# Kernel optimization log

Hardware: AMD Instinct MI355X
Metric: run time of the kernel (lower is better)

## Reference

```python
import jax, jax.numpy as jnp
import numpy as np

NDIGIT = 10
DIM_IN = 256
DIM_OUT = 784
BATCH = 16384


def setup_inputs() -> dict:
    key = jax.random.key(0)
    k_theta, k_label, k_W = jax.random.split(key, 3)
    theta = jax.random.normal(k_theta, (BATCH, DIM_IN), dtype=jnp.float32)
    label = jax.random.randint(k_label, (BATCH,), 0, NDIGIT, dtype=jnp.int32)
    # xavier_uniform for each (dim_out, dim_in) matrix
    limit = float(np.sqrt(6.0 / (DIM_IN + DIM_OUT)))
    megaW = jax.random.uniform(k_W, (NDIGIT, DIM_OUT, DIM_IN), dtype=jnp.float32,
                               minval=-limit, maxval=limit)
    megab = jnp.zeros((NDIGIT, DIM_OUT), dtype=jnp.float32)
    return {"theta": theta, "label": label, "megaW": megaW, "megab": megab}


def reference(theta, label, megaW, megab):
    # Dense compute across all 10 digit experts (matches torch.bmm over repeated theta)
    # added: [b, ndigit, dim_out]
    added = jnp.einsum('ndi,bi->bnd', megaW, theta) + megab[None, :, :]
    # Select the expert output per example by label (vector_gather)
    selected = jnp.take_along_axis(added, label[:, None, None].astype(jnp.int32), axis=1)[:, 0, :]
    probs = jax.nn.sigmoid(selected)
    return probs
```

## Files before the change

### kernel.cpp

```cpp
#include <hip/hip_runtime.h>
#include <hip/hip_bf16.h>

#define NDIGIT 10
#define DIM_IN 256
#define DIM_OUT 784
#define BATCH 16384
#define BM 64
#define BN 112
#define NCB 7
#define MAX_MT (BATCH / BM + NDIGIT)
#define GEMM_BLOCKS (MAX_MT * NCB)
#define QBYTES 14336

#define WS_IDX 1024
#define WS_WBF_BYTES 69632
#define WS_TH_BYTES (WS_WBF_BYTES + 2007040 * 2)
#define WS_NEED_OLD (WS_TH_BYTES)
#define WS_NEED_NEW (WS_TH_BYTES + BATCH * DIM_IN * 2)

typedef __attribute__((ext_vector_type(4))) float f32x4;
typedef __attribute__((ext_vector_type(8))) short bf16x8;

__device__ __forceinline__ short f2bf(float f) {
    union { float f; unsigned u; } c; c.f = f;
    unsigned u = c.u;
    u += 0x7fffu + ((u >> 16) & 1u);
    return (short)(u >> 16);
}

__device__ __forceinline__ void gload16(const void* gp, void* lp) {
    __builtin_amdgcn_global_load_lds(
        (const __attribute__((address_space(1))) void*)gp,
        (__attribute__((address_space(3))) void*)lp, 16, 0, 0);
}

__global__ void prep_k(const float* __restrict__ megaW,
                       const int* __restrict__ label,
                       int* __restrict__ wsi,
                       short* __restrict__ wbf) {
    int b = blockIdx.x, t = threadIdx.x;
    if (b < 980) {
        int base = b * 2048 + t * 8;
        f32x4 v0 = *(const f32x4*)(megaW + base);
        f32x4 v1 = *(const f32x4*)(megaW + base + 4);
        bf16x8 o;
        o[0] = f2bf(v0[0]); o[1] = f2bf(v0[1]); o[2] = f2bf(v0[2]); o[3] = f2bf(v0[3]);
        o[4] = f2bf(v1[0]); o[5] = f2bf(v1[1]); o[6] = f2bf(v1[2]); o[7] = f2bf(v1[3]);
        *(bf16x8*)(wbf + base) = o;
    } else {
        __shared__ int h[NDIGIT];
        int j = b - 980;
        if (t < NDIGIT) h[t] = 0;
        __syncthreads();
        int i0 = j * 512;
        atomicAdd(&h[label[i0 + t]], 1);
        atomicAdd(&h[label[i0 + 256 + t]], 1);
        __syncthreads();
        if (t < NDIGIT) wsi[64 + j * 16 + t] = h[t];
    }
}

__global__ void scatter2_k(const int* __restrict__ label, int* __restrict__ wsi) {
    __shared__ int tot[NDIGIT], bef[NDIGIT], base[NDIGIT + 1], cur[NDIGIT];
    int j = blockIdx.x, t = threadIdx.x;
    if (t < NDIGIT) {
        int s = 0, sb = 0;
        for (int jj = 0; jj < 32; ++jj) {
            int v = wsi[64 + jj * 16 + t];
            s += v;
            if (jj < j) sb += v;
        }
        tot[t] = s; bef[t] = sb;
    }
    __syncthreads();
    if (t == 0) {
        int off = 0;
        for (int g = 0; g < NDIGIT; ++g) { base[g] = off; off += tot[g]; }
        base[NDIGIT] = off;
    }
    __syncthreads();
    if (t < NDIGIT) cur[t] = base[t] + bef[t];
    __syncthreads();
    int i = j * 512 + t;
    int g = label[i];
    int r = atomicAdd(&cur[g], 1);
    wsi[WS_IDX + r] = i;
    if (j == 0 && t == 0) {
        int off = 0, toff = 0;
        for (int g2 = 0; g2 < NDIGIT; ++g2) {
            wsi[g2] = off; wsi[12 + g2] = toff;
            off += tot[g2]; toff += (tot[g2] + BM - 1) / BM;
        }
        wsi[10] = off; wsi[22] = toff; wsi[24] = toff;
    }
}

__global__ void gth_k(const float* __restrict__ theta,
                      const int* __restrict__ wsi,
                      short* __restrict__ thsort) {
    int gid = blockIdx.x * 256 + threadIdx.x;
    int r = gid >> 5;
    int c8 = (gid & 31) << 3;
    int src = wsi[WS_IDX + r];
    const float* p = theta + (size_t)src * DIM_IN + c8;
    f32x4 v0 = *(const f32x4*)p;
    f32x4 v1 = *(const f32x4*)(p + 4);
    bf16x8 o;
    o[0] = f2bf(v0[0]); o[1] = f2bf(v0[1]); o[2] = f2bf(v0[2]); o[3] = f2bf(v0[3]);
    o[4] = f2bf(v1[0]); o[5] = f2bf(v1[1]); o[6] = f2bf(v1[2]); o[7] = f2bf(v1[3]);
    *(bf16x8*)(thsort + (size_t)r * DIM_IN + c8) = o;
}

__device__ __forceinline__ void stage_q(const char* Wcb, int q, char* Bq, int tid) {
#pragma unroll
    for (int it = 0; it < 4; ++it) {
        int chunk = it * 256 + tid;
        if (chunk >= 896) chunk -= 128;
        int lbyte = chunk << 4;
        int L = lbyte ^ ((((lbyte >> 7) & 7)) << 4);
        int row = L >> 7, koff = L & 127;
        gload16(Wcb + row * 512 + q * 128 + koff, Bq + lbyte);
    }
}

#define COMPUTE(Q, BUF) do { \
    _Pragma("unroll") \
    for (int ksl = 0; ksl < 2; ++ksl) { \
        _Pragma("unroll") \
        for (int ns = 0; ns < NCB; ++ns) { \
            int n = ns * 16 + r16; \
            int byte = (n << 7) + (ksl << 6) + (kg << 4); \
            byte ^= (n & 7) << 4; \
            bf16x8 bfr = *(const bf16x8*)((const char*)(BUF) + byte); \
            acc[ns] = __builtin_amdgcn_mfma_f32_16x16x32_bf16(a[(Q) * 2 + ksl], bfr, acc[ns], 0, 0, 0); \
        } \
    } \
} while (0)

__launch_bounds__(256, 4)
__global__ void moe_gemm5_k(const short* __restrict__ thsort,
                            const float* __restrict__ megab,
                            const int* __restrict__ wsi,
                            const short* __restrict__ wbf,
                            float* __restrict__ out) {
    __shared__ char Bs0[QBYTES];
    __shared__ char Bs1[QBYTES];

    int Bid = blockIdx.x;
    const int q8 = GEMM_BLOCKS / 8, r8 = GEMM_BLOCKS % 8;
    int xcd = Bid & 7, slot = Bid >> 3;
    int w = (xcd < r8 ? xcd * (q8 + 1) : r8 * (q8 + 1) + (xcd - r8) * q8) + slot;
    int mt = w / NCB, cb = w % NCB;

    int total = wsi[24];
    if (mt >= total) return;

    int g = 0;
    while (mt >= wsi[12 + g + 1]) ++g;
    int lt    = mt - wsi[12 + g];
    int start = wsi[g];
    int cnt   = wsi[g + 1] - start;
    int row0  = lt * BM;
    int rc    = min(BM, cnt - row0);

    int tid = threadIdx.x;
    int wv = tid >> 6, l = tid & 63, r16 = l & 15, kg = l >> 4;

    int arow = start + row0 + wv * 16 + r16;
    if (arow > BATCH - 1) arow = BATCH - 1;
    const short* Ar = thsort + (size_t)arow * DIM_IN + kg * 8;
    bf16x8 a[8];
#pragma unroll
    for (int ks = 0; ks < 8; ++ks)
        a[ks] = *(const bf16x8*)(Ar + ks * 32);

    const int* idxlist = wsi + WS_IDX + start + row0;
    int rbase = wv * 16 + kg * 4;
    int orow[4];
#pragma unroll
    for (int j = 0; j < 4; ++j)
        orow[j] = (rbase + j < rc) ? idxlist[rbase + j] : -1;

    const char* Wcb = (const char*)(wbf + ((size_t)g * DIM_OUT + (size_t)cb * BN) * DIM_IN);

    stage_q(Wcb, 0, Bs0, tid);
    stage_q(Wcb, 1, Bs1, tid);

    f32x4 acc[NCB];
#pragma unroll
    for (int ns = 0; ns < NCB; ++ns) acc[ns] = (f32x4){0.f, 0.f, 0.f, 0.f};

    asm volatile("s_waitcnt vmcnt(4)" ::: "memory");
    __builtin_amdgcn_s_barrier();
    __builtin_amdgcn_sched_barrier(0);

    COMPUTE(0, Bs0);
    asm volatile("s_waitcnt lgkmcnt(0)" ::: "memory");
    __builtin_amdgcn_s_barrier();
    stage_q(Wcb, 2, Bs0, tid);
    asm volatile("s_waitcnt vmcnt(4)" ::: "memory");
    __builtin_amdgcn_s_barrier();
    __builtin_amdgcn_sched_barrier(0);

    COMPUTE(1, Bs1);
    asm volatile("s_waitcnt lgkmcnt(0)" ::: "memory");
    __builtin_amdgcn_s_barrier();
    stage_q(Wcb, 3, Bs1, tid);
    asm volatile("s_waitcnt vmcnt(4)" ::: "memory");
    __builtin_amdgcn_s_barrier();
    __builtin_amdgcn_sched_barrier(0);

    COMPUTE(2, Bs0);
    asm volatile("s_waitcnt lgkmcnt(0) vmcnt(0)" ::: "memory");
    __builtin_amdgcn_s_barrier();
    __builtin_amdgcn_sched_barrier(0);

    COMPUTE(3, Bs1);

    const float* bg = megab + (size_t)g * DIM_OUT + (size_t)cb * BN;
#pragma unroll
    for (int ns = 0; ns < NCB; ++ns) {
        int nloc = ns * 16 + r16;
        float bias = bg[nloc];
#pragma unroll
        for (int j = 0; j < 4; ++j) {
            if (orow[j] >= 0) {
                float x = acc[ns][j] + bias;
                out[(size_t)orow[j] * DIM_OUT + cb * BN + nloc] = 1.0f / (1.0f + __expf(-x));
            }
        }
    }
}

__launch_bounds__(256, 4)
__global__ void moe_gemm4_k(const float* __restrict__ theta,
                            const float* __restrict__ megab,
                            const int* __restrict__ wsi,
                            const short* __restrict__ wbf,
                            float* __restrict__ out) {
    __shared__ short Bsf[BN * 128];
    int Bid = blockIdx.x;
    const int q8 = GEMM_BLOCKS / 8, r8 = GEMM_BLOCKS % 8;
    int xcd = Bid & 7, slot = Bid >> 3;
    int w = (xcd < r8 ? xcd * (q8 + 1) : r8 * (q8 + 1) + (xcd - r8) * q8) + slot;
    int mt = w / NCB, cb = w % NCB;
    int total = wsi[24];
    if (mt >= total) return;
    int g = 0;
    while (mt >= wsi[12 + g + 1]) ++g;
    int lt    = mt - wsi[12 + g];
    int start = wsi[g];
    int cnt   = wsi[g + 1] - start;
    int row0  = lt * BM;
    int rc    = min(BM, cnt - row0);
    int tid = threadIdx.x;
    int wv = tid >> 6, l = tid & 63, r16 = l & 15, kg = l >> 4;
    const char* Wcb = (const char*)(wbf + ((size_t)g * DIM_OUT + (size_t)cb * BN) * DIM_IN);
#pragma unroll
    for (int it = 0; it < 7; ++it) {
        int lbyte = (it * 256 + tid) << 4;
        int L = lbyte ^ (((lbyte >> 8) & 7) << 4);
        int srcoff = ((L >> 8) << 9) + (L & 255);
        gload16(Wcb + srcoff, (char*)Bsf + lbyte);
    }
    const int* idxlist = wsi + WS_IDX + start + row0;
    int mloc = wv * 16 + r16;
    int asrc = (mloc < rc) ? idxlist[mloc] : idxlist[0];
    const float* Arow = (const float*)0;
    Arow = theta + (size_t)asrc * DIM_IN;
    bf16x8 a[8];
#pragma unroll
    for (int ks = 0; ks < 8; ++ks) {
        int k0 = ks * 32 + kg * 8;
        f32x4 v0 = *(const f32x4*)(Arow + k0);
        f32x4 v1 = *(const f32x4*)(Arow + k0 + 4);
        bf16x8 af;
        af[0] = f2bf(v0[0]); af[1] = f2bf(v0[1]);
        af[2] = f2bf(v0[2]); af[3] = f2bf(v0[3]);
        af[4] = f2bf(v1[0]); af[5] = f2bf(v1[1]);
        af[6] = f2bf(v1[2]); af[7] = f2bf(v1[3]);
        a[ks] = af;
    }
    f32x4 acc[NCB];
#pragma unroll
    for (int ns = 0; ns < NCB; ++ns) acc[ns] = (f32x4){0.f, 0.f, 0.f, 0.f};
    __syncthreads();
#pragma unroll
    for (int ks = 0; ks < 4; ++ks)
#pragma unroll
        for (int ns = 0; ns < NCB; ++ns) {
            int n = ns * 16 + r16;
            int byte = (n << 8) + (ks << 6) + (kg << 4);
            byte ^= (n & 7) << 4;
            bf16x8 b = *(const bf16x8*)((const char*)Bsf + byte);
            acc[ns] = __builtin_amdgcn_mfma_f32_16x16x32_bf16(a[ks], b, acc[ns], 0, 0, 0);
        }
    __syncthreads();
#pragma unroll
    for (int it = 0; it < 7; ++it) {
        int lbyte = (it * 256 + tid) << 4;
        int L = lbyte ^ (((lbyte >> 8) & 7) << 4);
        int srcoff = ((L >> 8) << 9) + (L & 255) + 256;
        gload16(Wcb + srcoff, (char*)Bsf + lbyte);
    }
    __syncthreads();
#pragma unroll
    for (int ks = 0; ks < 4; ++ks)
#pragma unroll
        for (int ns = 0; ns < NCB; ++ns) {
            int n = ns * 16 + r16;
            int byte = (n << 8) + (ks << 6) + (kg << 4);
            byte ^= (n & 7) << 4;
            bf16x8 b = *(const bf16x8*)((const char*)Bsf + byte);
            acc[ns] = __builtin_amdgcn_mfma_f32_16x16x32_bf16(a[4 + ks], b, acc[ns], 0, 0, 0);
        }
    const float* bg = megab + (size_t)g * DIM_OUT + (size_t)cb * BN;
    int rbase = wv * 16 + kg * 4;
    int orow[4];
#pragma unroll
    for (int j = 0; j < 4; ++j)
        orow[j] = (rbase + j < rc) ? idxlist[rbase + j] : -1;
#pragma unroll
    for (int ns = 0; ns < NCB; ++ns) {
        int nloc = ns * 16 + r16;
        float bias = bg[nloc];
#pragma unroll
        for (int j = 0; j < 4; ++j) {
            if (orow[j] >= 0) {
                float x = acc[ns][j] + bias;
                out[(size_t)orow[j] * DIM_OUT + cb * BN + nloc] = 1.0f / (1.0f + __expf(-x));
            }
        }
    }
}

extern "C" void kernel_launch(void* const* d_in, const int* in_sizes, int n_in,
                              void* d_out, int out_size, void* d_ws, size_t ws_size,
                              hipStream_t stream) {
    const float* theta = (const float*)d_in[0];
    const int*   label = (const int*)d_in[1];
    const float* megaW = (const float*)d_in[2];
    const float* megab = (const float*)d_in[3];
    float* out = (float*)d_out;
    int* wsi = (int*)d_ws;
    short* wbf = (short*)((char*)d_ws + WS_WBF_BYTES);

    prep_k    <<<1012, 256, 0, stream>>>(megaW, label, wsi, wbf);
    scatter2_k<<<32, 512, 0, stream>>>(label, wsi);

    if (ws_size >= (size_t)WS_NEED_NEW) {
        short* thsort = (short*)((char*)d_ws + WS_TH_BYTES);
        gth_k     <<<2048, 256, 0, stream>>>(theta, wsi, thsort);
        moe_gemm5_k<<<GEMM_BLOCKS, 256, 0, stream>>>(thsort, megab, wsi, wbf, out);
    } else {
        moe_gemm4_k<<<GEMM_BLOCKS, 256, 0, stream>>>(theta, megab, wsi, wbf, out);
    }
}
```

Measured before the change: 47.19 us.

## Precompute per-tile descriptors and simplify GEMM LDS staging schedule

The scatter kernel now writes a packed per-M-tile descriptor (start row, row count, expert id), so each GEMM block does one load instead of a serial search over expert tile offsets. The GEMM kernel drops the hand-tuned interleaved waitcnt and barrier pipeline. It now stages two K-quarters, computes both, syncs, then stages and computes the last two. The weight staging is issued before the A-fragment loads to overlap them. This trades finer-grained load/compute overlap for fewer barriers and simpler code, with some risk of exposed memory latency in the second half.

```diff
diff --git a/kernel.cpp b/kernel.cpp
--- a/kernel.cpp
+++ b/kernel.cpp
@@ -9,14 +9,14 @@
 #define BN 112
 #define NCB 7
 #define MAX_MT (BATCH / BM + NDIGIT)
-#define GEMM_BLOCKS (MAX_MT * NCB)
-#define QBYTES 14336
+#define G_BLOCKS (MAX_MT * NCB)
+#define QB 14336
 
 #define WS_IDX 1024
+#define WS_DESC 600
 #define WS_WBF_BYTES 69632
 #define WS_TH_BYTES (WS_WBF_BYTES + 2007040 * 2)
-#define WS_NEED_OLD (WS_TH_BYTES)
-#define WS_NEED_NEW (WS_TH_BYTES + BATCH * DIM_IN * 2)
+#define WS_NEED (WS_TH_BYTES + BATCH * DIM_IN * 2)
 
 typedef __attribute__((ext_vector_type(4))) float f32x4;
 typedef __attribute__((ext_vector_type(8))) short bf16x8;
@@ -61,7 +61,7 @@
 }
 
 __global__ void scatter2_k(const int* __restrict__ label, int* __restrict__ wsi) {
-    __shared__ int tot[NDIGIT], bef[NDIGIT], base[NDIGIT + 1], cur[NDIGIT];
+    __shared__ int tot[NDIGIT], bef[NDIGIT], base[NDIGIT + 1], cur[NDIGIT], toff[NDIGIT + 1];
     int j = blockIdx.x, t = threadIdx.x;
     if (t < NDIGIT) {
         int s = 0, sb = 0;
@@ -74,25 +74,34 @@
     }
     __syncthreads();
     if (t == 0) {
-        int off = 0;
-        for (int g = 0; g < NDIGIT; ++g) { base[g] = off; off += tot[g]; }
-        base[NDIGIT] = off;
+        int off = 0, tf = 0;
+        for (int g = 0; g < NDIGIT; ++g) {
+            base[g] = off; toff[g] = tf;
+            off += tot[g]; tf += (tot[g] + BM - 1) / BM;
+        }
+        base[NDIGIT] = off; toff[NDIGIT] = tf;
     }
     __syncthreads();
     if (t < NDIGIT) cur[t] = base[t] + bef[t];
+    if (j == 0) {
+        int ptotal = toff[NDIGIT];
+        for (int p = t; p < ptotal; p += 512) {
+            int g2 = 0;
+            while (p >= toff[g2 + 1]) ++g2;
+            int row0 = (p - toff[g2]) * BM;
+            int rcv = tot[g2] - row0; if (rcv > BM) rcv = BM;
+            wsi[WS_DESC + p] = (base[g2] + row0) | (rcv << 14) | (g2 << 21);
+        }
+        if (t < NDIGIT) { wsi[t] = base[t]; wsi[12 + t] = toff[t]; }
+        if (t == 0) {
+            wsi[10] = base[NDIGIT]; wsi[22] = toff[NDIGIT]; wsi[24] = toff[NDIGIT];
+        }
+    }
     __syncthreads();
     int i = j * 512 + t;
     int g = label[i];
     int r = atomicAdd(&cur[g], 1);
     wsi[WS_IDX + r] = i;
-    if (j == 0 && t == 0) {
-        int off = 0, toff = 0;
-        for (int g2 = 0; g2 < NDIGIT; ++g2) {
-            wsi[g2] = off; wsi[12 + g2] = toff;
-            off += tot[g2]; toff += (tot[g2] + BM - 1) / BM;
-        }
-        wsi[10] = off; wsi[22] = toff; wsi[24] = toff;
-    }
 }
 
 __global__ void gth_k(const float* __restrict__ theta,
@@ -123,31 +132,31 @@
     }
 }
 
-#define COMPUTE(Q, BUF) do { \
-    _Pragma("unroll") \
-    for (int ksl = 0; ksl < 2; ++ksl) { \
-        _Pragma("unroll") \
-        for (int ns = 0; ns < NCB; ++ns) { \
-            int n = ns * 16 + r16; \
-            int byte = (n << 7) + (ksl << 6) + (kg << 4); \
-            byte ^= (n & 7) << 4; \
-            bf16x8 bfr = *(const bf16x8*)((const char*)(BUF) + byte); \
-            acc[ns] = __builtin_amdgcn_mfma_f32_16x16x32_bf16(a[(Q) * 2 + ksl], bfr, acc[ns], 0, 0, 0); \
-        } \
-    } \
+#define COMPUTE_Q(Q, BUF) do {                                                 \
+    _Pragma("unroll")                                                          \
+    for (int ksl = 0; ksl < 2; ++ksl) {                                        \
+        _Pragma("unroll")                                                      \
+        for (int ns = 0; ns < NCB; ++ns) {                                     \
+            int n_ = ns * 16 + r16;                                            \
+            int byte_ = (n_ << 7) + (ksl << 6) + (kg << 4);                    \
+            byte_ ^= (n_ & 7) << 4;                                            \
+            bf16x8 bfr_ = *(const bf16x8*)((const char*)(BUF) + byte_);        \
+            acc[ns] = __builtin_amdgcn_mfma_f32_16x16x32_bf16(                 \
+                a[(Q) * 2 + ksl], bfr_, acc[ns], 0, 0, 0);                     \
+        }                                                                      \
+    }                                                                          \
 } while (0)
 
 __launch_bounds__(256, 4)
-__global__ void moe_gemm5_k(const short* __restrict__ thsort,
-                            const float* __restrict__ megab,
-                            const int* __restrict__ wsi,
-                            const short* __restrict__ wbf,
-                            float* __restrict__ out) {
-    __shared__ char Bs0[QBYTES];
-    __shared__ char Bs1[QBYTES];
+__global__ void moe_gemm10_k(const short* __restrict__ thsort,
+                             const float* __restrict__ megab,
+                             const int* __restrict__ wsi,
+                             const short* __restrict__ wbf,
+                             float* __restrict__ out) {
+    __shared__ char Bs[2 * QB];
 
     int Bid = blockIdx.x;
-    const int q8 = GEMM_BLOCKS / 8, r8 = GEMM_BLOCKS % 8;
+    const int q8 = G_BLOCKS / 8, r8 = G_BLOCKS % 8;
     int xcd = Bid & 7, slot = Bid >> 3;
     int w = (xcd < r8 ? xcd * (q8 + 1) : r8 * (q8 + 1) + (xcd - r8) * q8) + slot;
     int mt = w / NCB, cb = w % NCB;
@@ -155,69 +164,49 @@
     int total = wsi[24];
     if (mt >= total) return;
 
-    int g = 0;
-    while (mt >= wsi[12 + g + 1]) ++g;
-    int lt    = mt - wsi[12 + g];
-    int start = wsi[g];
-    int cnt   = wsi[g + 1] - start;
-    int row0  = lt * BM;
-    int rc    = min(BM, cnt - row0);
+    int d = wsi[WS_DESC + mt];
+    int startRow = d & 0x3FFF;
+    int rc = (d >> 14) & 0x7F;
+    int g  = d >> 21;
 
     int tid = threadIdx.x;
     int wv = tid >> 6, l = tid & 63, r16 = l & 15, kg = l >> 4;
 
-    int arow = start + row0 + wv * 16 + r16;
-    if (arow > BATCH - 1) arow = BATCH - 1;
-    const short* Ar = thsort + (size_t)arow * DIM_IN + kg * 8;
+    const char* Wcb = (const char*)(wbf + ((size_t)g * DIM_OUT + (size_t)cb * BN) * DIM_IN);
+
+    stage_q(Wcb, 0, Bs, tid);
+    stage_q(Wcb, 1, Bs + QB, tid);
+
+    int mloc = wv * 16 + r16; if (mloc >= rc) mloc = rc - 1;
+    const short* Ar = thsort + (size_t)(startRow + mloc) * DIM_IN + kg * 8;
     bf16x8 a[8];
 #pragma unroll
     for (int ks = 0; ks < 8; ++ks)
         a[ks] = *(const bf16x8*)(Ar + ks * 32);
 
-    const int* idxlist = wsi + WS_IDX + start + row0;
+    f32x4 acc[NCB];
+#pragma unroll
+    for (int ns = 0; ns < NCB; ++ns) acc[ns] = (f32x4){0.f, 0.f, 0.f, 0.f};
+
+    __syncthreads();
+    COMPUTE_Q(0, Bs);
+    COMPUTE_Q(1, Bs + QB);
+    __syncthreads();
+
+    stage_q(Wcb, 2, Bs, tid);
+    stage_q(Wcb, 3, Bs + QB, tid);
+    __syncthreads();
+    COMPUTE_Q(2, Bs);
+    COMPUTE_Q(3, Bs + QB);
+
+    const float* bg = megab + (size_t)g * DIM_OUT + (size_t)cb * BN;
+    const int* idxl = wsi + WS_IDX + startRow;
     int rbase = wv * 16 + kg * 4;
     int orow[4];
 #pragma unroll
     for (int j = 0; j < 4; ++j)
-        orow[j] = (rbase + j < rc) ? idxlist[rbase + j] : -1;
-
-    const char* Wcb = (const char*)(wbf + ((size_t)g * DIM_OUT + (size_t)cb * BN) * DIM_IN);
-
-    stage_q(Wcb, 0, Bs0, tid);
-    stage_q(Wcb, 1, Bs1, tid);
-
-    f32x4 acc[NCB];
-#pragma unroll
-    for (int ns = 0; ns < NCB; ++ns) acc[ns] = (f32x4){0.f, 0.f, 0.f, 0.f};
-
-    asm volatile("s_waitcnt vmcnt(4)" ::: "memory");
-    __builtin_amdgcn_s_barrier();
-    __builtin_amdgcn_sched_barrier(0);
-
-    COMPUTE(0, Bs0);
-    asm volatile("s_waitcnt lgkmcnt(0)" ::: "memory");
-    __builtin_amdgcn_s_barrier();
-    stage_q(Wcb, 2, Bs0, tid);
-    asm volatile("s_waitcnt vmcnt(4)" ::: "memory");
-    __builtin_amdgcn_s_barrier();
-    __builtin_amdgcn_sched_barrier(0);
-
-    COMPUTE(1, Bs1);
-    asm volatile("s_waitcnt lgkmcnt(0)" ::: "memory");
-    __builtin_amdgcn_s_barrier();
-    stage_q(Wcb, 3, Bs1, tid);
-    asm volatile("s_waitcnt vmcnt(4)" ::: "memory");
-    __builtin_amdgcn_s_barrier();
-    __builtin_amdgcn_sched_barrier(0);
-
-    COMPUTE(2, Bs0);
-    asm volatile("s_waitcnt lgkmcnt(0) vmcnt(0)" ::: "memory");
-    __builtin_amdgcn_s_barrier();
-    __builtin_amdgcn_sched_barrier(0);
-
-    COMPUTE(3, Bs1);
-
-    const float* bg = megab + (size_t)g * DIM_OUT + (size_t)cb * BN;
+        orow[j] = (rbase + j < rc) ? idxl[rbase + j] : -1;
+
 #pragma unroll
     for (int ns = 0; ns < NCB; ++ns) {
         int nloc = ns * 16 + r16;
@@ -240,7 +229,7 @@
                             float* __restrict__ out) {
     __shared__ short Bsf[BN * 128];
     int Bid = blockIdx.x;
-    const int q8 = GEMM_BLOCKS / 8, r8 = GEMM_BLOCKS % 8;
+    const int q8 = G_BLOCKS / 8, r8 = G_BLOCKS % 8;
     int xcd = Bid & 7, slot = Bid >> 3;
     int w = (xcd < r8 ? xcd * (q8 + 1) : r8 * (q8 + 1) + (xcd - r8) * q8) + slot;
     int mt = w / NCB, cb = w % NCB;
@@ -266,8 +255,7 @@
     const int* idxlist = wsi + WS_IDX + start + row0;
     int mloc = wv * 16 + r16;
     int asrc = (mloc < rc) ? idxlist[mloc] : idxlist[0];
-    const float* Arow = (const float*)0;
-    Arow = theta + (size_t)asrc * DIM_IN;
+    const float* Arow = theta + (size_t)asrc * DIM_IN;
     bf16x8 a[8];
 #pragma unroll
     for (int ks = 0; ks < 8; ++ks) {
@@ -348,11 +336,11 @@
     prep_k    <<<1012, 256, 0, stream>>>(megaW, label, wsi, wbf);
     scatter2_k<<<32, 512, 0, stream>>>(label, wsi);
 
-    if (ws_size >= (size_t)WS_NEED_NEW) {
+    if (ws_size >= (size_t)WS_NEED) {
         short* thsort = (short*)((char*)d_ws + WS_TH_BYTES);
-        gth_k     <<<2048, 256, 0, stream>>>(theta, wsi, thsort);
-        moe_gemm5_k<<<GEMM_BLOCKS, 256, 0, stream>>>(thsort, megab, wsi, wbf, out);
+        gth_k      <<<2048, 256, 0, stream>>>(theta, wsi, thsort);
+        moe_gemm10_k<<<G_BLOCKS, 256, 0, stream>>>(thsort, megab, wsi, wbf, out);
     } else {
-        moe_gemm4_k<<<GEMM_BLOCKS, 256, 0, stream>>>(theta, megab, wsi, wbf, out);
-    }
-}
+        moe_gemm4_k<<<G_BLOCKS, 256, 0, stream>>>(theta, megab, wsi, wbf, out);
+    }
+}
```

Result: no change. 47.25 us (+0.1%).
